# Performance work log

Measured on AMD Instinct MI355X. Metric: run time of the kernel, lower is better.

## Reference

```python
import jax, jax.numpy as jnp
import numpy as np

# xLSTM '80k' config: 4 blocks (mLSTM at 0,2,3; sLSTM at 1)
B, S, F = 128, 256, 10      # batch, seq (= context_length = forecast_horizon), features
E, NH = 40, 8               # d_model, heads
DH = E // NH                # 5,  sLSTM per-head dim
I = 128                     # mLSTM inner dim = round64(2*E)
QKB = 4; NQK = I // QKB     # q/k/v block-diagonal proj: 32 blocks of 4
MDH = I // NH               # 16, mLSTM per-head dim
FFD = 64                    # gated FFN dim = round64(1.3*E)
K = 4                       # causal conv kernel
NMB = 3                     # number of mLSTM blocks


def layer_norm(x, w, eps=1e-5):
    mu = x.mean(-1, keepdims=True)
    return (x - mu) * jax.lax.rsqrt(x.var(-1, keepdims=True) + eps) * w


def multihead_norm(x, w, nh, eps=1e-5):
    # per-head group norm over D//nh channels, weight only
    b, s, d = x.shape
    xh = x.reshape(b, s, nh, d // nh)
    xh = (xh - xh.mean(-1, keepdims=True)) * jax.lax.rsqrt(xh.var(-1, keepdims=True) + eps)
    return xh.reshape(b, s, d) * w


def causal_conv(x, w, b):
    # depthwise causal conv1d, kernel K; x: (B,S,C), w: (C,K)
    xt = x.transpose(0, 2, 1)
    y = jax.lax.conv_general_dilated(xt, w[:, None, :], (1,), [(K - 1, 0)],
                                     feature_group_count=x.shape[-1],
                                     dimension_numbers=('NCH', 'OIH', 'NCH'))
    return (y + b[None, :, None]).transpose(0, 2, 1)


def headwise(x, w):
    # block-diagonal linear (LinearHeadwiseExpand, no bias): w (nb, bo, bi)
    nb, bo, bi = w.shape
    xh = x.reshape(*x.shape[:-1], nb, bi)
    return jnp.einsum('bsni,noi->bsno', xh, w).reshape(*x.shape[:-1], nb * bo)


def pos_encoding():
    pos = jnp.arange(S, dtype=jnp.float32)[:, None]
    div = jnp.exp(jnp.arange(0, E, 2, dtype=jnp.float32) * (-np.log(10000.0) / E))
    pe = jnp.zeros((S, E), jnp.float32)
    pe = pe.at[:, 0::2].set(jnp.sin(pos * div))
    pe = pe.at[:, 1::2].set(jnp.cos(pos * div))
    return pe


def mlstm_layer(x, up_w, conv_w, conv_b, q_w, k_w, v_w, ig_w, ig_b, fg_w, fg_b, mhn_w, skip, down_w):
    x_m, z = jnp.split(x @ up_w.T, 2, axis=-1)                 # each (B,S,I)
    x_c = jax.nn.silu(causal_conv(x_m, conv_w, conv_b))
    q, k, v = headwise(x_c, q_w), headwise(x_c, k_w), headwise(x_m, v_w)
    gin = jnp.concatenate([q, k, v], axis=-1)                   # (B,S,3I)
    ip = (gin @ ig_w.T + ig_b).transpose(0, 2, 1)               # (B,NH,S)
    fp = (gin @ fg_w.T + fg_b).transpose(0, 2, 1)
    heads = lambda t: t.reshape(B, S, NH, MDH).transpose(0, 2, 1, 3)
    qh, kh, vh = heads(q), heads(k), heads(v)
    # stabilized parallel mLSTM (parallel_stabilized_simple)
    Fc = jnp.cumsum(jax.nn.log_sigmoid(fp), axis=-1)
    log_fg = Fc[..., :, None] - Fc[..., None, :]                # (B,NH,S,S)
    mask = jnp.tril(jnp.ones((S, S), bool))
    log_D = jnp.where(mask, log_fg, -jnp.inf) + ip[..., None, :]
    mD = jnp.max(log_D, axis=-1, keepdims=True)
    D = jnp.exp(log_D - mD)
    qk = jnp.einsum('bhsd,bhtd->bhst', qh, kh) * (MDH ** -0.5)
    C = qk * D
    nrm = jnp.maximum(jnp.abs(C.sum(-1, keepdims=True)), jnp.exp(-mD))
    h = jnp.einsum('bhst,bhtd->bhsd', C / (nrm + 1e-6), vh)
    h = multihead_norm(h.transpose(0, 2, 1, 3).reshape(B, S, I), mhn_w, NH)
    return ((h + skip * x_c) * jax.nn.silu(z)) @ down_w.T


def slstm_layer(x, conv_w, conv_b, wi, wf, wz, wo, R, bias, mhn_w):
    x_c = jax.nn.silu(causal_conv(x, conv_w, conv_b))
    g = lambda inp, w: headwise(inp, w).reshape(B, S, NH, DH)
    # i,f from conv path; z,o from raw input (order i,f,z,o)
    gx = jnp.stack([g(x_c, wi), g(x_c, wf), g(x, wz), g(x, wo)], axis=3)  # (B,S,NH,4,DH)
    gx = gx.transpose(1, 0, 2, 3, 4)                                      # (S,B,NH,4,DH)

    def step(carry, g_t):
        h, c, n, m = carry
        raw = g_t + jnp.einsum('bhd,hgde->bhge', h, R) + bias
        i_r, f_r, z_r, o_r = raw[:, :, 0], raw[:, :, 1], raw[:, :, 2], raw[:, :, 3]
        logfplusm = m + jax.nn.log_sigmoid(f_r)
        m_new = jnp.maximum(i_r, logfplusm)
        ig, fg = jnp.exp(i_r - m_new), jnp.exp(logfplusm - m_new)
        c_new = fg * c + ig * jnp.tanh(z_r)
        n_new = fg * n + ig
        h_new = jax.nn.sigmoid(o_r) * c_new / n_new
        return (h_new, c_new, n_new, m_new), h_new

    z0 = jnp.zeros((B, NH, DH), jnp.float32)
    _, hs = jax.lax.scan(step, (z0, z0, z0, z0), gx)
    return multihead_norm(hs.transpose(1, 0, 2, 3).reshape(B, S, E), mhn_w, NH)


def _forward(x, in_proj_w, in_proj_b, m_ln_w, m_up_w, m_conv_w, m_conv_b, m_q_w, m_k_w, m_v_w,
             m_ig_w, m_ig_b, m_fg_w, m_fg_b, m_mhn_w, m_skip, m_down_w,
             s_ln1_w, s_conv_w, s_conv_b, s_wi, s_wf, s_wz, s_wo, s_R, s_b, s_mhn_w,
             s_ln2_w, s_ff_up_w, s_ff_down_w, post_ln_w, out_w, out_b):
    h = x @ in_proj_w.T + in_proj_b + pos_encoding()
    mb = lambda h, j: h + mlstm_layer(layer_norm(h, m_ln_w[j]), m_up_w[j], m_conv_w[j], m_conv_b[j],
                                      m_q_w[j], m_k_w[j], m_v_w[j], m_ig_w[j], m_ig_b[j],
                                      m_fg_w[j], m_fg_b[j], m_mhn_w[j], m_skip[j], m_down_w[j])
    h = mb(h, 0)                       # block 0: mLSTM
    # block 1: sLSTM + gated FFN (pre-LN residual)
    h = h + slstm_layer(layer_norm(h, s_ln1_w), s_conv_w, s_conv_b, s_wi, s_wf, s_wz, s_wo, s_R, s_b, s_mhn_w)
    gpre, up = jnp.split(layer_norm(h, s_ln2_w) @ s_ff_up_w.T, 2, axis=-1)
    h = h + (jax.nn.gelu(gpre, approximate=False) * up) @ s_ff_down_w.T
    h = mb(h, 1)                       # block 2: mLSTM
    h = mb(h, 2)                       # block 3: mLSTM
    return layer_norm(h, post_ln_w) @ out_w.T + out_b


def setup_inputs():
    ks = iter(jax.random.split(jax.random.key(0), 64))
    rn = lambda shape, fan: jax.random.normal(next(ks), shape, jnp.float32) * (fan ** -0.5)
    d = {}
    d['x'] = jax.random.normal(next(ks), (B, S, F), jnp.float32)
    d['in_proj_w'] = rn((E, F), F); d['in_proj_b'] = jnp.zeros((E,), jnp.float32)
    d['m_ln_w'] = jnp.ones((NMB, E), jnp.float32)
    d['m_up_w'] = rn((NMB, 2 * I, E), E)
    d['m_conv_w'] = rn((NMB, I, K), K); d['m_conv_b'] = jnp.zeros((NMB, I), jnp.float32)
    d['m_q_w'] = rn((NMB, NQK, QKB, QKB), QKB)
    d['m_k_w'] = rn((NMB, NQK, QKB, QKB), QKB)
    d['m_v_w'] = rn((NMB, NQK, QKB, QKB), QKB)
    d['m_ig_w'] = rn((NMB, NH, 3 * I), 3 * I); d['m_ig_b'] = jnp.zeros((NMB, NH), jnp.float32)
    d['m_fg_w'] = rn((NMB, NH, 3 * I), 3 * I); d['m_fg_b'] = 3.0 * jnp.ones((NMB, NH), jnp.float32)
    d['m_mhn_w'] = jnp.ones((NMB, I), jnp.float32); d['m_skip'] = jnp.ones((NMB, I), jnp.float32)
    d['m_down_w'] = rn((NMB, E, I), I)
    d['s_ln1_w'] = jnp.ones((E,), jnp.float32)
    d['s_conv_w'] = rn((E, K), K); d['s_conv_b'] = jnp.zeros((E,), jnp.float32)
    d['s_wi'] = rn((NH, DH, DH), DH); d['s_wf'] = rn((NH, DH, DH), DH)
    d['s_wz'] = rn((NH, DH, DH), DH); d['s_wo'] = rn((NH, DH, DH), DH)
    d['s_R'] = rn((NH, 4, DH, DH), DH); d['s_b'] = jnp.zeros((NH, 4, DH), jnp.float32)
    d['s_mhn_w'] = jnp.ones((E,), jnp.float32); d['s_ln2_w'] = jnp.ones((E,), jnp.float32)
    d['s_ff_up_w'] = rn((2 * FFD, E), E); d['s_ff_down_w'] = rn((E, FFD), FFD)
    d['post_ln_w'] = jnp.ones((E,), jnp.float32)
    d['out_w'] = rn((1, E), E); d['out_b'] = jnp.zeros((1,), jnp.float32)
    return d


def reference(x, in_proj_w, in_proj_b, m_ln_w, m_up_w, m_conv_w, m_conv_b, m_q_w, m_k_w, m_v_w,
              m_ig_w, m_ig_b, m_fg_w, m_fg_b, m_mhn_w, m_skip, m_down_w,
              s_ln1_w, s_conv_w, s_conv_b, s_wi, s_wf, s_wz, s_wo, s_R, s_b, s_mhn_w,
              s_ln2_w, s_ff_up_w, s_ff_down_w, post_ln_w, out_w, out_b):
    return _forward(x, in_proj_w, in_proj_b, m_ln_w, m_up_w, m_conv_w, m_conv_b, m_q_w, m_k_w, m_v_w,
                    m_ig_w, m_ig_b, m_fg_w, m_fg_b, m_mhn_w, m_skip, m_down_w,
                    s_ln1_w, s_conv_w, s_conv_b, s_wi, s_wf, s_wz, s_wo, s_R, s_b, s_mhn_w,
                    s_ln2_w, s_ff_up_w, s_ff_down_w, post_ln_w, out_w, out_b)
```

## Files before the change

kernel.cpp:

```cpp
#include <hip/hip_runtime.h>
#include <math.h>

constexpr int cB = 128, cS = 256, cF = 10, cE = 40, cNH = 8, cDH = 5;
constexpr int cI = 128, cMDH = 16, cK = 4;

typedef __attribute__((ext_vector_type(8))) short short8v;
typedef __attribute__((ext_vector_type(4))) float f32x4;
typedef __attribute__((ext_vector_type(16))) float f32x16;

#define BC8(v, l) __uint_as_float(__builtin_amdgcn_ds_swizzle(__float_as_uint(v), ((l) << 5) | 0x18))

__device__ __forceinline__ short f2bf(float f) {
    unsigned u = __float_as_uint(f);
    u += 0x7FFF + ((u >> 16) & 1);
    return (short)(u >> 16);
}
__device__ __forceinline__ float bf2f(short s) {
    return __uint_as_float(((unsigned)(unsigned short)s) << 16);
}

__global__ __launch_bounds__(256) void init_k(const float* __restrict__ x, const float* __restrict__ w,
                                              const float* __restrict__ b, float* __restrict__ h) {
    int idx = blockIdx.x * 256 + threadIdx.x;
    int e = idx % cE; int bs = idx / cE; int s = bs % cS;
    float acc = b[e];
    const float* xr = x + (size_t)bs * cF;
#pragma unroll
    for (int f = 0; f < cF; ++f) acc += xr[f] * w[e * cF + f];
    int i2 = e >> 1;
    float div = expf(-(float)(2 * i2) * (logf(10000.f) / 40.0f));
    float arg = (float)s * div;
    acc += (e & 1) ? cosf(arg) : sinf(arg);
    h[idx] = acc;
}

__global__ __launch_bounds__(256) void ln_up_k(const float* __restrict__ h, const float* __restrict__ lnw,
                                               const float* __restrict__ upw, float* __restrict__ xmz) {
    __shared__ float lnr[16][cE];
    __shared__ float wT[cE * 257];
    int row0 = blockIdx.x * 16;
    int tid = threadIdx.x;
    for (int j = tid; j < 2560; j += 256) {
        float4 v = ((const float4*)upw)[j];
        int o = j / 10, kq = (j - o * 10) * 4;
        wT[(kq + 0) * 257 + o] = v.x;
        wT[(kq + 1) * 257 + o] = v.y;
        wT[(kq + 2) * 257 + o] = v.z;
        wT[(kq + 3) * 257 + o] = v.w;
    }
    if (tid < 16) {
        const float* r = h + (size_t)(row0 + tid) * cE;
        float mu = 0.f;
        for (int k = 0; k < cE; ++k) mu += r[k];
        mu *= (1.f / cE);
        float va = 0.f;
        for (int k = 0; k < cE; ++k) { float d = r[k] - mu; va += d * d; }
        va *= (1.f / cE);
        float rs = rsqrtf(va + 1e-5f);
        for (int k = 0; k < cE; ++k) lnr[tid][k] = (r[k] - mu) * rs * lnw[k];
    }
    __syncthreads();
    int o = tid;
    float acc[16];
#pragma unroll
    for (int r = 0; r < 16; ++r) acc[r] = 0.f;
    for (int k = 0; k < cE; ++k) {
        float wv = wT[k * 257 + o];
#pragma unroll
        for (int r = 0; r < 16; ++r) acc[r] = fmaf(lnr[r][k], wv, acc[r]);
    }
#pragma unroll
    for (int r = 0; r < 16; ++r) xmz[(size_t)(row0 + r) * 256 + o] = acc[r];
}

template <int C>
__global__ __launch_bounds__(256) void conv_silu_k(const float* __restrict__ in, int instride,
                                                   const float* __restrict__ w, const float* __restrict__ bias,
                                                   float* __restrict__ out) {
    int idx = blockIdx.x * 256 + threadIdx.x;
    int c = idx % C; int bs = idx / C; int s = bs % cS;
    float acc = bias[c];
#pragma unroll
    for (int j = 0; j < cK; ++j) {
        int sj = s - 3 + j;
        if (sj >= 0) acc += in[(size_t)(bs + j - 3) * instride + c] * w[c * cK + j];
    }
    float sg = 1.f / (1.f + __expf(-acc));
    out[idx] = acc * sg;
}

__global__ __launch_bounds__(256) void conv_silu_bf_k(const float* __restrict__ in,
                                                      const float* __restrict__ w, const float* __restrict__ bias,
                                                      short* __restrict__ out) {
    int idx = blockIdx.x * 256 + threadIdx.x;
    int c = idx & 127; int bs = idx >> 7; int s = bs & 255;
    float acc = bias[c];
#pragma unroll
    for (int j = 0; j < cK; ++j) {
        int sj = s - 3 + j;
        if (sj >= 0) acc += in[(size_t)(bs + j - 3) * 256 + c] * w[c * cK + j];
    }
    float sg = 1.f / (1.f + __expf(-acc));
    out[idx] = f2bf(acc * sg);
}

__global__ __launch_bounds__(256) void qkv_k(const short* __restrict__ xc, const float* __restrict__ xmz,
                                             const float* __restrict__ qw, const float* __restrict__ kw,
                                             const float* __restrict__ vw,
                                             short* __restrict__ qb, short* __restrict__ kb, short* __restrict__ vb) {
    int idx = blockIdx.x * 256 + threadIdx.x;
    int c = idx & 127; int bs = idx >> 7;
    int n = c >> 2, o = c & 3;
    const short* xcr = xc + (size_t)bs * cI + n * 4;
    const float* xmr = xmz + (size_t)bs * 256 + n * 4;
    const float* qwp = qw + n * 16 + o * 4;
    const float* kwp = kw + n * 16 + o * 4;
    const float* vwp = vw + n * 16 + o * 4;
    float aq = 0, ak = 0, av = 0;
#pragma unroll
    for (int i = 0; i < 4; ++i) {
        float a = bf2f(xcr[i]), m = xmr[i];
        aq += a * qwp[i]; ak += a * kwp[i]; av += m * vwp[i];
    }
    qb[idx] = f2bf(aq); kb[idx] = f2bf(ak); vb[idx] = f2bf(av);
}

__global__ __launch_bounds__(256, 2) void gates_k(const short* __restrict__ qb, const short* __restrict__ kb,
                                                  const short* __restrict__ vb, const float* __restrict__ igw,
                                                  const float* __restrict__ igb, const float* __restrict__ fgw,
                                                  const float* __restrict__ fgb,
                                                  float* __restrict__ ipb, float* __restrict__ fpb) {
    __shared__ float g[32 * 388];
    __shared__ float w[16 * 388];
    int row0 = blockIdx.x * 32;
    int tid = threadIdx.x;

    for (int i = tid; i < 16 * 96; i += 256) {
        int r = i / 96, c4 = i - r * 96;
        const float* src = (r < 8) ? (igw + r * 384) : (fgw + (r - 8) * 384);
        *(float4*)&w[r * 388 + c4 * 4] = ((const float4*)src)[c4];
    }
    for (int i = tid; i < 32 * 48; i += 256) {
        int r = i / 48, c8 = i - r * 48;
        size_t gr = (size_t)(row0 + r) * cI;
        const short8v* src = (c8 < 16) ? (const short8v*)(qb + gr) + c8
                           : (c8 < 32) ? (const short8v*)(kb + gr) + (c8 - 16)
                                       : (const short8v*)(vb + gr) + (c8 - 32);
        short8v v = *src;
        float* dst = &g[r * 388 + c8 * 8];
#pragma unroll
        for (int j = 0; j < 8; ++j) dst[j] = bf2f(v[j]);
    }
    __syncthreads();

    int rp = tid >> 3;
    int hp = tid & 7;
    int o0 = 2 * hp, o1 = o0 + 1;

    const float4* gp = (const float4*)(g + rp * 388);
    const float4* w0p = (const float4*)(w + o0 * 388);
    const float4* w1p = (const float4*)(w + o1 * 388);

    float a0e = 0.f, a0o = 0.f, a1e = 0.f, a1o = 0.f;
#pragma unroll 2
    for (int c4 = 0; c4 < 96; c4 += 2) {
        float4 gv0 = gp[c4], gv1 = gp[c4 + 1];
        float4 wa0 = w0p[c4], wa1 = w0p[c4 + 1];
        float4 wb0 = w1p[c4], wb1 = w1p[c4 + 1];
        a0e = fmaf(gv0.x, wa0.x, a0e); a0e = fmaf(gv0.y, wa0.y, a0e);
        a0e = fmaf(gv0.z, wa0.z, a0e); a0e = fmaf(gv0.w, wa0.w, a0e);
        a1e = fmaf(gv0.x, wb0.x, a1e); a1e = fmaf(gv0.y, wb0.y, a1e);
        a1e = fmaf(gv0.z, wb0.z, a1e); a1e = fmaf(gv0.w, wb0.w, a1e);
        a0o = fmaf(gv1.x, wa1.x, a0o); a0o = fmaf(gv1.y, wa1.y, a0o);
        a0o = fmaf(gv1.z, wa1.z, a0o); a0o = fmaf(gv1.w, wa1.w, a0o);
        a1o = fmaf(gv1.x, wb1.x, a1o); a1o = fmaf(gv1.y, wb1.y, a1o);
        a1o = fmaf(gv1.z, wb1.z, a1o); a1o = fmaf(gv1.w, wb1.w, a1o);
    }
    float a0 = a0e + a0o, a1 = a1e + a1o;

    int h0 = o0 & 7, wch0 = o0 >> 3;
    int h1 = o1 & 7, wch1 = o1 >> 3;
    float b0 = wch0 ? fgb[h0] : igb[h0];
    float b1 = wch1 ? fgb[h1] : igb[h1];
    int grow = row0 + rp;
    int bb = grow >> 8, ss = grow & 255;
    float* d0 = (wch0 ? fpb : ipb) + (size_t)(bb * cNH + h0) * cS + ss;
    float* d1 = (wch1 ? fpb : ipb) + (size_t)(bb * cNH + h1) * cS + ss;
    *d0 = a0 + b0; *d1 = a1 + b1;
}

constexpr int QKW = 24;
constexpr int VTW = 264;
constexpr int CBW = 40;

__global__ __launch_bounds__(256, 3) void attn_k(const short* __restrict__ qg, const short* __restrict__ kg,
                                                 const short* __restrict__ vg, const float* __restrict__ ipg,
                                                 const float* __restrict__ fpg, short* __restrict__ hatt) {
    int bh = blockIdx.x; int b = bh >> 3, h = bh & 7;
    int tid = threadIdx.x;
    int wid = tid >> 6, lane = tid & 63;
    int colL = lane & 15, grp = lane >> 4;
    int col32 = lane & 31, hi = lane >> 5;

    __shared__ float sEA[cS], sEMx[cS], sFlr[cS];
    __shared__ short sQ[cS * QKW], sK[cS * QKW];
    __shared__ short sVt[cMDH * VTW];
    __shared__ short sCb[4][32 * CBW];
    __shared__ float sSum[4][32];

    {
        const float4 fp4 = ((const float4*)(fpg + (size_t)bh * cS))[lane];
        const float4 ip4 = ((const float4*)(ipg + (size_t)bh * cS))[lane];
        float fpa[4] = {fp4.x, fp4.y, fp4.z, fp4.w};
        float ipa[4] = {ip4.x, ip4.y, ip4.z, ip4.w};
        float p[4];
        float run = 0.f;
#pragma unroll
        for (int i = 0; i < 4; ++i) {
            float xx = fpa[i];
            float lsg = fminf(xx, 0.f) - log1pf(expf(-fabsf(xx)));
            run += lsg; p[i] = run;
        }
        float cum = p[3];
#pragma unroll
        for (int off = 1; off < 64; off <<= 1) { float t = __shfl_up(cum, off); if (lane >= off) cum += t; }
        float excl = cum - p[3];
        float aa[4], fcv4[4];
#pragma unroll
        for (int i = 0; i < 4; ++i) {
            fcv4[i] = excl + p[i];
            aa[i] = ipa[i] - fcv4[i];
            sEA[lane * 4 + i] = __expf(aa[i]);
        }
        float mq[4]; mq[0] = aa[0];
#pragma unroll
        for (int i = 1; i < 4; ++i) mq[i] = fmaxf(mq[i - 1], aa[i]);
        float cm = mq[3];
#pragma unroll
        for (int off = 1; off < 64; off <<= 1) { float t = __shfl_up(cm, off); if (lane >= off) cm = fmaxf(cm, t); }
        float exm = __shfl_up(cm, 1);
        if (lane == 0) exm = -3.0e38f;
#pragma unroll
        for (int i = 0; i < 4; ++i) {
            float Mx = fmaxf(exm, mq[i]);
            sEMx[lane * 4 + i] = 0.25f * __expf(-Mx);
            sFlr[lane * 4 + i] = __expf(-(fcv4[i] + Mx));
        }
    }

    {
        int t = tid;
        const short8v* qp = (const short8v*)(qg + ((size_t)(b * cS) + t) * cI + h * cMDH);
        const short8v* kp = (const short8v*)(kg + ((size_t)(b * cS) + t) * cI + h * cMDH);
        const short8v* vp = (const short8v*)(vg + ((size_t)(b * cS) + t) * cI + h * cMDH);
        *(short8v*)(sQ + t * QKW) = qp[0];
        *(short8v*)(sQ + t * QKW + 8) = qp[1];
        *(short8v*)(sK + t * QKW) = kp[0];
        *(short8v*)(sK + t * QKW + 8) = kp[1];
        short8v v0 = vp[0], v1 = vp[1];
#pragma unroll
        for (int d = 0; d < 8; ++d) sVt[d * VTW + t] = v0[d];
#pragma unroll
        for (int d = 0; d < 8; ++d) sVt[(8 + d) * VTW + t] = v1[d];
    }
    __syncthreads();

    short* Cb = sCb[wid];
    float* Sm = sSum[wid];
    const int tiles2[2] = {wid, 7 - wid};

    for (int sti = 0; sti < 2; ++sti) {
        int st = tiles2[sti];
        int s0 = st * 32;

        short8v aQ = *(const short8v*)(sQ + (s0 + col32) * QKW + hi * 8);
        int r16[16]; float eMx16[16];
#pragma unroll
        for (int reg = 0; reg < 16; ++reg) {
            int r = (reg & 3) + 8 * (reg >> 2) + 4 * hi;
            r16[reg] = r;
            eMx16[reg] = sEMx[s0 + r];
        }
        float sum16[16];
#pragma unroll
        for (int reg = 0; reg < 16; ++reg) sum16[reg] = 0.f;
        f32x4 hacc0 = {0.f, 0.f, 0.f, 0.f}, hacc1 = {0.f, 0.f, 0.f, 0.f};

        for (int tt = 0; tt <= st; ++tt) {
            int t0 = tt * 32;
            short8v bK = *(const short8v*)(sK + (t0 + col32) * QKW + hi * 8);
            f32x16 zz = {0.f, 0.f, 0.f, 0.f, 0.f, 0.f, 0.f, 0.f,
                         0.f, 0.f, 0.f, 0.f, 0.f, 0.f, 0.f, 0.f};
            f32x16 d = __builtin_amdgcn_mfma_f32_32x32x16_bf16(aQ, bK, zz, 0, 0, 0);
            float ea = sEA[t0 + col32];
            bool diag = (tt == st);
#pragma unroll
            for (int reg = 0; reg < 16; ++reg) {
                float v = d[reg] * (ea * eMx16[reg]);
                if (diag && col32 > r16[reg]) v = 0.f;
                sum16[reg] += v;
                Cb[r16[reg] * CBW + col32] = f2bf(v);
            }
            short8v bV  = *(const short8v*)(sVt + colL * VTW + t0 + grp * 8);
            short8v aC0 = *(const short8v*)(Cb + colL * CBW + grp * 8);
            hacc0 = __builtin_amdgcn_mfma_f32_16x16x32_bf16(aC0, bV, hacc0, 0, 0, 0);
            short8v aC1 = *(const short8v*)(Cb + (16 + colL) * CBW + grp * 8);
            hacc1 = __builtin_amdgcn_mfma_f32_16x16x32_bf16(aC1, bV, hacc1, 0, 0, 0);
        }

#pragma unroll
        for (int reg = 0; reg < 16; ++reg) {
            float s = sum16[reg];
#pragma unroll
            for (int m = 1; m < 32; m <<= 1) s += __shfl_xor(s, m);
            sum16[reg] = s;
        }
        if (col32 == 0) {
#pragma unroll
            for (int reg = 0; reg < 16; ++reg) Sm[r16[reg]] = sum16[reg];
        }

#pragma unroll
        for (int sub = 0; sub < 2; ++sub) {
            f32x4 hacc = sub ? hacc1 : hacc0;
#pragma unroll
            for (int j = 0; j < 4; ++j) {
                int rloc = sub * 16 + grp * 4 + j;
                int sr = s0 + rloc;
                float sC = Sm[rloc];
                float nrm = fmaxf(fabsf(sC), sFlr[sr]) + 1e-6f;
                hatt[((size_t)(b * cS) + sr) * cI + h * cMDH + colL] = f2bf(hacc[j] / nrm);
            }
        }
    }
}

__global__ __launch_bounds__(320) void down_mhn_k(const short* __restrict__ hatt, const short* __restrict__ xc,
                                                  const float* __restrict__ xmz, const float* __restrict__ mhnw,
                                                  const float* __restrict__ skip, const float* __restrict__ dw,
                                                  float* __restrict__ h) {
    __shared__ float yl[8 * 128];
    int row0 = blockIdx.x * 8;
    int tid = threadIdx.x;
    for (int i = tid; i < 128; i += 320) {
        short8v v = ((const short8v*)(hatt + (size_t)row0 * cI))[i];
        float* dst = &yl[i * 8];
#pragma unroll
        for (int j = 0; j < 8; ++j) dst[j] = bf2f(v[j]);
    }
    __syncthreads();
    if (tid < 64) {
        int r = tid >> 3, hh = tid & 7;
        int row = row0 + r;
        float* g = yl + r * 128 + hh * 16;
        float xv[16];
        float mu = 0.f;
#pragma unroll
        for (int d = 0; d < 16; ++d) { xv[d] = g[d]; mu += xv[d]; }
        mu *= (1.f / 16);
        float va = 0.f;
#pragma unroll
        for (int d = 0; d < 16; ++d) { float dd = xv[d] - mu; va += dd * dd; }
        va *= (1.f / 16);
        float rs = rsqrtf(va + 1e-5f);
        const short* xcr = xc + (size_t)row * cI + hh * 16;
        const float* zr  = xmz + (size_t)row * 256 + 128 + hh * 16;
#pragma unroll
        for (int d = 0; d < 16; ++d) {
            int i = hh * 16 + d;
            float z = zr[d];
            float sg = 1.f / (1.f + __expf(-z));
            g[d] = ((xv[d] - mu) * rs * mhnw[i] + skip[i] * bf2f(xcr[d])) * (z * sg);
        }
    }
    __syncthreads();
    int r = tid / 40, e = tid % 40;
    const float* dr = dw + e * cI;
    const float* yr = yl + r * cI;
    float acc = 0.f;
    for (int i = 0; i < cI; ++i) acc += yr[i] * dr[i];
    h[(size_t)(row0 + r) * cE + e] += acc;
}

__global__ __launch_bounds__(256) void ln_rows_k(const float* __restrict__ h, const float* __restrict__ w,
                                                 float* __restrict__ out) {
    int rid = blockIdx.x * 256 + threadIdx.x;
    const float* r = h + (size_t)rid * cE;
    float mu = 0;
    for (int k = 0; k < cE; ++k) mu += r[k];
    mu *= (1.f / cE);
    float va = 0;
    for (int k = 0; k < cE; ++k) { float d = r[k] - mu; va += d * d; }
    va *= (1.f / cE);
    float rs = rsqrtf(va + 1e-5f);
    float* o = out + (size_t)rid * cE;
    for (int k = 0; k < cE; ++k) o[k] = (r[k] - mu) * rs * w[k];
}

__global__ __launch_bounds__(256) void sgates_k(const float* __restrict__ xcs, const float* __restrict__ ln1,
                                                const float* __restrict__ wi, const float* __restrict__ wf,
                                                const float* __restrict__ wz, const float* __restrict__ wo,
                                                float* __restrict__ gall) {
    int idx = blockIdx.x * 256 + threadIdx.x;
    int g = idx & 3; int r1 = idx >> 2;
    int e = r1 % 5; int r2 = r1 / 5;
    int bh = r2 & 1023; int s = r2 >> 10;
    int b = bh >> 3, h = bh & 7;
    const float* in = (g < 2) ? xcs : ln1;
    const float* w = (g == 0) ? wi : (g == 1) ? wf : (g == 2) ? wz : wo;
    const float* ir = in + ((size_t)(b * cS) + s) * cE + h * cDH;
    const float* wp = w + h * 25 + e * 5;
    float acc = 0.f;
#pragma unroll
    for (int i = 0; i < 5; ++i) acc += ir[i] * wp[i];
    gall[idx] = acc;
}

__global__ __launch_bounds__(64) void scan_k(const float* __restrict__ gall, const float* __restrict__ R,
                                             const float* __restrict__ bias, const float* __restrict__ mhnw,
                                             float* __restrict__ hbuf) {
    int lane = threadIdx.x;
    int grp = lane >> 3;
    int e = lane & 7;
    int ee = e < 5 ? e : 4;
    int bh = blockIdx.x * 8 + grp;
    int h = bh & 7;

    __shared__ float sOut[8][1285];

    float Rr[4][5];
#pragma unroll
    for (int g = 0; g < 4; ++g)
#pragma unroll
        for (int d = 0; d < 5; ++d) Rr[g][d] = R[h * 100 + g * 25 + d * 5 + ee];
    float bg[4];
#pragma unroll
    for (int g = 0; g < 4; ++g) bg[g] = bias[h * 20 + g * 5 + ee];
    float wmh = mhnw[h * 5 + ee];

    const float4* gp = (const float4*)gall + ((size_t)bh * 5 + ee);

    float4 rg[16];
#pragma unroll
    for (int j = 0; j < 16; ++j) rg[j] = gp[(size_t)j * 5120];

    float cstate = 0.f, nstate = 0.f, mstate = 0.f;
    float hs0 = 0.f, hs1 = 0.f, hs2 = 0.f, hs3 = 0.f, hs4 = 0.f;

    for (int t = 0; t < cS; t += 16) {
#pragma unroll
        for (int j = 0; j < 16; ++j) {
            float4 g4 = rg[j];
            rg[j] = gp[(size_t)(t + j + 16) * 5120];

            float ir = g4.x + bg[0], fr = g4.y + bg[1], zr = g4.z + bg[2], orr = g4.w + bg[3];
            ir = fmaf(hs0, Rr[0][0], ir); fr = fmaf(hs0, Rr[1][0], fr);
            zr = fmaf(hs0, Rr[2][0], zr); orr = fmaf(hs0, Rr[3][0], orr);
            ir = fmaf(hs1, Rr[0][1], ir); fr = fmaf(hs1, Rr[1][1], fr);
            zr = fmaf(hs1, Rr[2][1], zr); orr = fmaf(hs1, Rr[3][1], orr);
            ir = fmaf(hs2, Rr[0][2], ir); fr = fmaf(hs2, Rr[1][2], fr);
            zr = fmaf(hs2, Rr[2][2], zr); orr = fmaf(hs2, Rr[3][2], orr);
            ir = fmaf(hs3, Rr[0][3], ir); fr = fmaf(hs3, Rr[1][3], fr);
            zr = fmaf(hs3, Rr[2][3], zr); orr = fmaf(hs3, Rr[3][3], orr);
            ir = fmaf(hs4, Rr[0][4], ir); fr = fmaf(hs4, Rr[1][4], fr);
            zr = fmaf(hs4, Rr[2][4], zr); orr = fmaf(hs4, Rr[3][4], orr);

            float lsg = fminf(fr, 0.f) - __logf(1.f + __expf(-fabsf(fr)));
            float lfm = mstate + lsg;
            float mn = fmaxf(ir, lfm);
            float ig = __expf(ir - mn), fg = __expf(lfm - mn);
            float th = 1.f - 2.f * __builtin_amdgcn_rcpf(__expf(2.f * zr) + 1.f);
            float cn = fg * cstate + ig * th;
            float nn = fg * nstate + ig;
            float sg = __builtin_amdgcn_rcpf(1.f + __expf(-orr));
            float hn = sg * cn * __builtin_amdgcn_rcpf(nn);
            cstate = cn; nstate = nn; mstate = mn;

            hs0 = BC8(hn, 0); hs1 = BC8(hn, 1); hs2 = BC8(hn, 2);
            hs3 = BC8(hn, 3); hs4 = BC8(hn, 4);
            float mu = ((hs0 + hs1) + (hs2 + hs3) + hs4) * 0.2f;
            float d0 = hs0 - mu, d1 = hs1 - mu, d2 = hs2 - mu, d3 = hs3 - mu, d4 = hs4 - mu;
            float va = (d0 * d0 + d1 * d1 + d2 * d2 + d3 * d3 + d4 * d4) * 0.2f;
            float rs = __builtin_amdgcn_rsqf(va + 1e-5f);
            if (e < 5) sOut[grp][(t + j) * 5 + e] = (hn - mu) * rs * wmh;
        }
    }
    __syncthreads();

    for (int i = lane; i < 8 * 1280; i += 64) {
        int c = i / 1280;
        int r = i - c * 1280;
        int tt = r / 5, e2 = r - tt * 5;
        int bh2 = blockIdx.x * 8 + c;
        int b2 = bh2 >> 3, h2 = bh2 & 7;
        float* hp = hbuf + ((size_t)b2 * cS + tt) * cE + h2 * cDH + e2;
        *hp += sOut[c][r];
    }
}

__global__ __launch_bounds__(256) void ff_k(float* __restrict__ h, const float* __restrict__ lnw,
                                            const float* __restrict__ upw, const float* __restrict__ dnw) {
    __shared__ float lnr[8][cE];
    __shared__ float ffr[8][64];
    int row0 = blockIdx.x * 8;
    int tid = threadIdx.x;
    if (tid < 8) {
        const float* r = h + (size_t)(row0 + tid) * cE;
        float mu = 0;
        for (int k = 0; k < cE; ++k) mu += r[k];
        mu *= (1.f / cE);
        float va = 0;
        for (int k = 0; k < cE; ++k) { float d = r[k] - mu; va += d * d; }
        va *= (1.f / cE);
        float rs = rsqrtf(va + 1e-5f);
        for (int k = 0; k < cE; ++k) lnr[tid][k] = (r[k] - mu) * rs * lnw[k];
    }
    __syncthreads();
    {
        int r = tid >> 5;
        int f0 = (tid & 31) * 2;
#pragma unroll
        for (int ff = 0; ff < 2; ++ff) {
            int f = f0 + ff;
            float a = 0, u = 0;
            const float* wa = upw + f * cE;
            const float* wu = upw + (64 + f) * cE;
            for (int k = 0; k < cE; ++k) {
                float xv = lnr[r][k];
                a = fmaf(xv, wa[k], a);
                u = fmaf(xv, wu[k], u);
            }
            float g = 0.5f * a * (1.f + erff(a * 0.70710678118f));
            ffr[r][f] = g * u;
        }
    }
    __syncthreads();
    for (int i = tid; i < 320; i += 256) {
        int r = i / 40, e = i - r * 40;
        const float* dr = dnw + e * 64;
        const float* fr = ffr[r];
        float acc = 0.f;
        for (int k = 0; k < 64; ++k) acc = fmaf(fr[k], dr[k], acc);
        h[(size_t)(row0 + r) * cE + e] += acc;
    }
}

__global__ __launch_bounds__(256) void final_k(const float* __restrict__ h, const float* __restrict__ lnw,
                                               const float* __restrict__ ow, const float* __restrict__ ob,
                                               float* __restrict__ out) {
    int rid = blockIdx.x * 256 + threadIdx.x;
    const float* r = h + (size_t)rid * cE;
    float mu = 0;
    for (int k = 0; k < cE; ++k) mu += r[k];
    mu *= (1.f / cE);
    float va = 0;
    for (int k = 0; k < cE; ++k) { float d = r[k] - mu; va += d * d; }
    va *= (1.f / cE);
    float rs = rsqrtf(va + 1e-5f);
    float acc = ob[0];
    for (int k = 0; k < cE; ++k) acc += (r[k] - mu) * rs * lnw[k] * ow[k];
    out[rid] = acc;
}

extern "C" void kernel_launch(void* const* d_in, const int* in_sizes, int n_in,
                              void* d_out, int out_size, void* d_ws, size_t ws_size,
                              hipStream_t stream) {
    const float* x        = (const float*)d_in[0];
    const float* in_w     = (const float*)d_in[1];
    const float* in_b     = (const float*)d_in[2];
    const float* m_ln_w   = (const float*)d_in[3];
    const float* m_up_w   = (const float*)d_in[4];
    const float* m_conv_w = (const float*)d_in[5];
    const float* m_conv_b = (const float*)d_in[6];
    const float* m_q_w    = (const float*)d_in[7];
    const float* m_k_w    = (const float*)d_in[8];
    const float* m_v_w    = (const float*)d_in[9];
    const float* m_ig_w   = (const float*)d_in[10];
    const float* m_ig_b   = (const float*)d_in[11];
    const float* m_fg_w   = (const float*)d_in[12];
    const float* m_fg_b   = (const float*)d_in[13];
    const float* m_mhn_w  = (const float*)d_in[14];
    const float* m_skip   = (const float*)d_in[15];
    const float* m_down_w = (const float*)d_in[16];
    const float* s_ln1_w  = (const float*)d_in[17];
    const float* s_conv_w = (const float*)d_in[18];
    const float* s_conv_b = (const float*)d_in[19];
    const float* s_wi     = (const float*)d_in[20];
    const float* s_wf     = (const float*)d_in[21];
    const float* s_wz     = (const float*)d_in[22];
    const float* s_wo     = (const float*)d_in[23];
    const float* s_R      = (const float*)d_in[24];
    const float* s_bias   = (const float*)d_in[25];
    const float* s_mhn_w  = (const float*)d_in[26];
    const float* s_ln2_w  = (const float*)d_in[27];
    const float* s_ff_up  = (const float*)d_in[28];
    const float* s_ff_dn  = (const float*)d_in[29];
    const float* post_ln_w= (const float*)d_in[30];
    const float* out_w    = (const float*)d_in[31];
    const float* out_b    = (const float*)d_in[32];

    float* ws   = (float*)d_ws;
    float* h    = ws;
    float* xmz  = h + 1310720;
    short* xcb  = (short*)(xmz + 8388608);
    short* qb   = xcb + 4194304;
    short* kb   = qb + 4194304;
    short* vb   = kb + 4194304;
    float* ipb  = (float*)(vb + 4194304);
    float* fpb  = ipb + 262144;
    short* hatt = (short*)(fpb + 262144);
    float* lnbuf = xmz;
    float* xcs   = xmz + 1310720;
    float* gall  = xmz + 2621440;

    init_k<<<5120, 256, 0, stream>>>(x, in_w, in_b, h);

    auto mlstm = [&](int j) {
        ln_up_k<<<2048, 256, 0, stream>>>(h, m_ln_w + j * cE, m_up_w + (size_t)j * 256 * cE, xmz);
        conv_silu_bf_k<<<16384, 256, 0, stream>>>(xmz, m_conv_w + j * cI * cK, m_conv_b + j * cI, xcb);
        qkv_k<<<16384, 256, 0, stream>>>(xcb, xmz, m_q_w + j * 512, m_k_w + j * 512, m_v_w + j * 512, qb, kb, vb);
        gates_k<<<1024, 256, 0, stream>>>(qb, kb, vb, m_ig_w + j * cNH * 384, m_ig_b + j * cNH,
                                          m_fg_w + j * cNH * 384, m_fg_b + j * cNH, ipb, fpb);
        attn_k<<<1024, 256, 0, stream>>>(qb, kb, vb, ipb, fpb, hatt);
        down_mhn_k<<<4096, 320, 0, stream>>>(hatt, xcb, xmz, m_mhn_w + j * cI, m_skip + j * cI,
                                             m_down_w + j * cE * cI, h);
    };

    mlstm(0);

    ln_rows_k<<<128, 256, 0, stream>>>(h, s_ln1_w, lnbuf);
    conv_silu_k<40><<<5120, 256, 0, stream>>>(lnbuf, 40, s_conv_w, s_conv_b, xcs);
    sgates_k<<<20480, 256, 0, stream>>>(xcs, lnbuf, s_wi, s_wf, s_wz, s_wo, gall);
    scan_k<<<128, 64, 0, stream>>>(gall, s_R, s_bias, s_mhn_w, h);

    ff_k<<<4096, 256, 0, stream>>>(h, s_ln2_w, s_ff_up, s_ff_dn);

    mlstm(1);
    mlstm(2);

    final_k<<<128, 256, 0, stream>>>(h, post_ln_w, out_w, out_b, (float*)d_out);
}
```

Before: 808.7 us.

## Use bf16 MFMA with hi/lo split weights for mLSTM gate projection

Replaces the scalar fp32 FMA gate projection with 16x16x32 bf16 MFMA instructions. A new preprocessing kernel splits the fp32 gate weights into bf16 high and low parts so accuracy stays close to fp32. Activations now stay in bf16 in shared memory, and each block handles 64 rows instead of 32. The cost is an extra kernel launch plus a second MFMA per k-chunk, and the output stores are strided across rows.

```diff
diff --git a/kernel.cpp b/kernel.cpp
--- a/kernel.cpp
+++ b/kernel.cpp
@@ -125,68 +125,74 @@
     qb[idx] = f2bf(aq); kb[idx] = f2bf(ak); vb[idx] = f2bf(av);
 }
 
+__global__ __launch_bounds__(256) void wsplit_k(const float* __restrict__ igw, const float* __restrict__ fgw,
+                                                short* __restrict__ wsp) {
+    int idx = blockIdx.x * 256 + threadIdx.x;
+    if (idx >= 3 * 32 * 392) return;
+    int j = idx / (32 * 392);
+    int rem = idx - j * (32 * 392);
+    int r = rem / 392, k = rem - r * 392;
+    int hl = r >> 4, o = r & 15;
+    short out = 0;
+    if (k < 384) {
+        const float* wsrc = (o < 8) ? (igw + ((size_t)j * 8 + o) * 384)
+                                    : (fgw + ((size_t)j * 8 + (o - 8)) * 384);
+        float w = wsrc[k];
+        short hi = f2bf(w);
+        out = (hl == 0) ? hi : f2bf(w - bf2f(hi));
+    }
+    wsp[idx] = out;
+}
+
+constexpr int GW = 392;
 __global__ __launch_bounds__(256, 2) void gates_k(const short* __restrict__ qb, const short* __restrict__ kb,
-                                                  const short* __restrict__ vb, const float* __restrict__ igw,
-                                                  const float* __restrict__ igb, const float* __restrict__ fgw,
-                                                  const float* __restrict__ fgb,
+                                                  const short* __restrict__ vb, const short* __restrict__ wsp,
+                                                  const float* __restrict__ igb, const float* __restrict__ fgb,
                                                   float* __restrict__ ipb, float* __restrict__ fpb) {
-    __shared__ float g[32 * 388];
-    __shared__ float w[16 * 388];
-    int row0 = blockIdx.x * 32;
+    __shared__ short sG[64 * GW];
+    __shared__ short sW[32 * GW];
+    int row0 = blockIdx.x * 64;
     int tid = threadIdx.x;
 
-    for (int i = tid; i < 16 * 96; i += 256) {
-        int r = i / 96, c4 = i - r * 96;
-        const float* src = (r < 8) ? (igw + r * 384) : (fgw + (r - 8) * 384);
-        *(float4*)&w[r * 388 + c4 * 4] = ((const float4*)src)[c4];
-    }
-    for (int i = tid; i < 32 * 48; i += 256) {
+    for (int i = tid; i < 32 * 49; i += 256) {
+        int r = i / 49, c8 = i - r * 49;
+        *(short8v*)&sW[r * GW + c8 * 8] = ((const short8v*)(wsp + r * GW))[c8];
+    }
+    for (int i = tid; i < 64 * 48; i += 256) {
         int r = i / 48, c8 = i - r * 48;
         size_t gr = (size_t)(row0 + r) * cI;
         const short8v* src = (c8 < 16) ? (const short8v*)(qb + gr) + c8
                            : (c8 < 32) ? (const short8v*)(kb + gr) + (c8 - 16)
                                        : (const short8v*)(vb + gr) + (c8 - 32);
-        short8v v = *src;
-        float* dst = &g[r * 388 + c8 * 8];
-#pragma unroll
-        for (int j = 0; j < 8; ++j) dst[j] = bf2f(v[j]);
-    }
-    __syncthreads();
-
-    int rp = tid >> 3;
-    int hp = tid & 7;
-    int o0 = 2 * hp, o1 = o0 + 1;
-
-    const float4* gp = (const float4*)(g + rp * 388);
-    const float4* w0p = (const float4*)(w + o0 * 388);
-    const float4* w1p = (const float4*)(w + o1 * 388);
-
-    float a0e = 0.f, a0o = 0.f, a1e = 0.f, a1o = 0.f;
-#pragma unroll 2
-    for (int c4 = 0; c4 < 96; c4 += 2) {
-        float4 gv0 = gp[c4], gv1 = gp[c4 + 1];
-        float4 wa0 = w0p[c4], wa1 = w0p[c4 + 1];
-        float4 wb0 = w1p[c4], wb1 = w1p[c4 + 1];
-        a0e = fmaf(gv0.x, wa0.x, a0e); a0e = fmaf(gv0.y, wa0.y, a0e);
-        a0e = fmaf(gv0.z, wa0.z, a0e); a0e = fmaf(gv0.w, wa0.w, a0e);
-        a1e = fmaf(gv0.x, wb0.x, a1e); a1e = fmaf(gv0.y, wb0.y, a1e);
-        a1e = fmaf(gv0.z, wb0.z, a1e); a1e = fmaf(gv0.w, wb0.w, a1e);
-        a0o = fmaf(gv1.x, wa1.x, a0o); a0o = fmaf(gv1.y, wa1.y, a0o);
-        a0o = fmaf(gv1.z, wa1.z, a0o); a0o = fmaf(gv1.w, wa1.w, a0o);
-        a1o = fmaf(gv1.x, wb1.x, a1o); a1o = fmaf(gv1.y, wb1.y, a1o);
-        a1o = fmaf(gv1.z, wb1.z, a1o); a1o = fmaf(gv1.w, wb1.w, a1o);
-    }
-    float a0 = a0e + a0o, a1 = a1e + a1o;
-
-    int h0 = o0 & 7, wch0 = o0 >> 3;
-    int h1 = o1 & 7, wch1 = o1 >> 3;
-    float b0 = wch0 ? fgb[h0] : igb[h0];
-    float b1 = wch1 ? fgb[h1] : igb[h1];
-    int grow = row0 + rp;
-    int bb = grow >> 8, ss = grow & 255;
-    float* d0 = (wch0 ? fpb : ipb) + (size_t)(bb * cNH + h0) * cS + ss;
-    float* d1 = (wch1 ? fpb : ipb) + (size_t)(bb * cNH + h1) * cS + ss;
-    *d0 = a0 + b0; *d1 = a1 + b1;
+        *(short8v*)&sG[r * GW + c8 * 8] = *src;
+    }
+    __syncthreads();
+
+    int wid = tid >> 6, lane = tid & 63;
+    int colL = lane & 15, grp = lane >> 4;
+    const short* gRow = sG + (wid * 16 + colL) * GW;
+    const short* wHi  = sW + colL * GW;
+    const short* wLo  = sW + (16 + colL) * GW;
+
+    f32x4 acc = {0.f, 0.f, 0.f, 0.f};
+    for (int kc = 0; kc < 12; ++kc) {
+        short8v a  = *(const short8v*)(gRow + kc * 32 + grp * 8);
+        short8v bh = *(const short8v*)(wHi + kc * 32 + grp * 8);
+        short8v bl = *(const short8v*)(wLo + kc * 32 + grp * 8);
+        acc = __builtin_amdgcn_mfma_f32_16x16x32_bf16(a, bh, acc, 0, 0, 0);
+        acc = __builtin_amdgcn_mfma_f32_16x16x32_bf16(a, bl, acc, 0, 0, 0);
+    }
+
+    int o = colL;
+    int hh = o & 7, wch = o >> 3;
+    float bias = wch ? fgb[hh] : igb[hh];
+    float* dst = wch ? fpb : ipb;
+#pragma unroll
+    for (int j = 0; j < 4; ++j) {
+        int grow = row0 + wid * 16 + grp * 4 + j;
+        int bb = grow >> 8, ss = grow & 255;
+        dst[(size_t)(bb * cNH + hh) * cS + ss] = acc[j] + bias;
+    }
 }
 
 constexpr int QKW = 24;
@@ -609,18 +615,20 @@
     float* ipb  = (float*)(vb + 4194304);
     float* fpb  = ipb + 262144;
     short* hatt = (short*)(fpb + 262144);
+    short* wsp  = hatt + 4194304;
     float* lnbuf = xmz;
     float* xcs   = xmz + 1310720;
     float* gall  = xmz + 2621440;
 
+    wsplit_k<<<147, 256, 0, stream>>>(m_ig_w, m_fg_w, wsp);
     init_k<<<5120, 256, 0, stream>>>(x, in_w, in_b, h);
 
     auto mlstm = [&](int j) {
         ln_up_k<<<2048, 256, 0, stream>>>(h, m_ln_w + j * cE, m_up_w + (size_t)j * 256 * cE, xmz);
         conv_silu_bf_k<<<16384, 256, 0, stream>>>(xmz, m_conv_w + j * cI * cK, m_conv_b + j * cI, xcb);
         qkv_k<<<16384, 256, 0, stream>>>(xcb, xmz, m_q_w + j * 512, m_k_w + j * 512, m_v_w + j * 512, qb, kb, vb);
-        gates_k<<<1024, 256, 0, stream>>>(qb, kb, vb, m_ig_w + j * cNH * 384, m_ig_b + j * cNH,
-                                          m_fg_w + j * cNH * 384, m_fg_b + j * cNH, ipb, fpb);
+        gates_k<<<512, 256, 0, stream>>>(qb, kb, vb, wsp + (size_t)j * 32 * GW,
+                                         m_ig_b + j * cNH, m_fg_b + j * cNH, ipb, fpb);
         attn_k<<<1024, 256, 0, stream>>>(qb, kb, vb, ipb, fpb, hatt);
         down_mhn_k<<<4096, 320, 0, stream>>>(hatt, xcb, xmz, m_mhn_w + j * cI, m_skip + j * cI,
                                              m_down_w + j * cE * cI, h);
```

Measured after the change: 776.7 us, median of 2. 4.0% less time.
